# Kernel tuning notes

Measured on AMD Instinct MI355X. Metric: run time of the kernel, lower is better.

The kernel has to match this reference:

```python
import jax, jax.numpy as jnp
import numpy as np
import math

N_NODES = 100000
N_EDGES = 1600000
IN_FEATS = 64
H_FEATS = 64
NUM_CLASSES = 2
LS_D = [2, 4, 6, 8]
LS_COEFF = [1.0, 1.0, 1.0, 1.0]
K = 4  # polynomial order per conv (len of each theta)


def _chi_theta(d, coeff):
    # Faithful port of calculate_theta_Chi for d > 0: fit chi-square-like
    # density on [0,2] with a degree-3 Chebyshev series, reverse coeffs.
    n = 2 * d
    m = 1.0 / (n / 2 + 1)  # i = n/2 - 1, m = 1/(i+2)
    def y(x):
        x = np.asarray(x, dtype=np.float64)
        return 1.0 / (2 ** (n / 2) * math.gamma(n / 2)) * (x / m) ** (n / 2 - 1) * np.exp(-(x / m) / 2)
    xs = np.linspace(0.0, 2.0, 20001)
    S = np.trapz(y(xs), xs)  # dense trapezoid ~ scipy.integrate.quad on [0,2]
    lambs = np.linspace(0.0, 2.0, 500)
    c = np.polynomial.chebyshev.chebfit(lambs, y(lambs) / S, 3)
    return (c[::-1] * coeff).astype(np.float32)

THETAS_NP = np.stack([_chi_theta(d, c) for d, c in zip(LS_D, LS_COEFF)])  # [4, K]


def setup_inputs() -> dict:
    key = jax.random.key(0)
    ks = jax.random.split(key, 8)
    sc = 0.05
    return {
        "x": jax.random.normal(ks[0], (N_NODES, IN_FEATS), dtype=jnp.float32),
        "src": jax.random.randint(ks[1], (N_EDGES,), 0, N_NODES, dtype=jnp.int32),
        "dst": jax.random.randint(ks[2], (N_EDGES,), 0, N_NODES, dtype=jnp.int32),
        "thetas": jnp.asarray(THETAS_NP),
        "W1": jax.random.normal(ks[3], (IN_FEATS, H_FEATS), dtype=jnp.float32) * sc,
        "b1": jnp.zeros((H_FEATS,), dtype=jnp.float32),
        "W2": jax.random.normal(ks[4], (H_FEATS, H_FEATS), dtype=jnp.float32) * sc,
        "b2": jnp.zeros((H_FEATS,), dtype=jnp.float32),
        "Wm1": jax.random.normal(ks[5], (H_FEATS * len(LS_D), H_FEATS), dtype=jnp.float32) * sc,
        "bm1": jnp.zeros((H_FEATS,), dtype=jnp.float32),
        "Wm2": jax.random.normal(ks[6], (H_FEATS, NUM_CLASSES), dtype=jnp.float32) * sc,
        "bm2": jnp.zeros((NUM_CLASSES,), dtype=jnp.float32),
    }


def reference(x, src, dst, thetas, W1, b1, W2, b2, Wm1, bm1, Wm2, bm2):
    n = x.shape[0]
    # input MLP stem
    h = jax.nn.relu(x @ W1 + b1)
    h = jax.nn.relu(h @ W2 + b2)
    # D^{-1/2} from in-degrees (clamped to >= 1), as in DGL in_degrees()
    deg = jax.ops.segment_sum(jnp.ones_like(dst, dtype=h.dtype), dst, num_segments=n)
    dinv = jnp.maximum(deg, 1.0) ** -0.5  # [N]
    dinv = dinv[:, None]  # [N, 1]
    # shared Laplacian power sequence: feats[k] = L^k h with L = I - D^-1/2 A D^-1/2
    feats = [h]
    f = h
    for _ in range(K - 1):
        t = f * dinv                                   # [N, H]
        agg = jax.ops.segment_sum(t[src], dst, num_segments=n)  # gather-scatter SpMM
        f = f - agg * dinv
        feats.append(f)
    F = jnp.stack(feats)  # [K, N, H]
    # per-conv polynomial combination, then concat along feature dim
    h_final = jnp.einsum('ck,knh->nch', thetas, F).reshape(n, -1)  # [N, C*H]
    # output MLP (2 layers)
    h_out = jax.nn.relu(h_final @ Wm1 + bm1)
    return h_out @ Wm2 + bm2
```

## Files before the change

### kernel.cpp

```cpp
#include <hip/hip_runtime.h>
#include <math.h>

#define TS  256
#define GS  192
#define BCAP2 4608
#define CHUNK 4096

typedef __attribute__((ext_vector_type(8))) short short8v;
typedef __attribute__((ext_vector_type(4))) float f32x4;

__device__ __forceinline__ unsigned short f2bf(float f) {
    unsigned int u = __builtin_bit_cast(unsigned int, f);
    u += 0x7fff + ((u >> 16) & 1);
    return (unsigned short)(u >> 16);
}
__device__ __forceinline__ float bf2f(unsigned short s) {
    return __builtin_bit_cast(float, ((unsigned int)s) << 16);
}
__device__ __forceinline__ void fma4(float4& a, float s, const float4& b) {
    a.x = fmaf(s, b.x, a.x);
    a.y = fmaf(s, b.y, a.y);
    a.z = fmaf(s, b.z, a.z);
    a.w = fmaf(s, b.w, a.w);
}

__global__ void zero_k(int* __restrict__ p, int n) {
    int i = blockIdx.x * blockDim.x + threadIdx.x;
    int st = gridDim.x * blockDim.x;
    for (; i < n; i += st) p[i] = 0;
}

__global__ __launch_bounds__(256) void part1_k(const int* __restrict__ src,
        const int* __restrict__ dst, int* __restrict__ gcnt,
        unsigned int* __restrict__ pairs, int E, int NB) {
    __shared__ int lcnt[512];
    __shared__ int lbase[512];
    __shared__ int lpos[512];
    int tid = threadIdx.x;
    int base = blockIdx.x * CHUNK;
    int m = E - base; if (m > CHUNK) m = CHUNK;
    for (int b = tid; b < NB; b += 256) { lcnt[b] = 0; lpos[b] = 0; }
    __syncthreads();
    for (int i = tid; i < m; i += 256)
        atomicAdd(&lcnt[dst[base + i] >> 8], 1);
    __syncthreads();
    for (int b = tid; b < NB; b += 256)
        lbase[b] = (lcnt[b] > 0) ? atomicAdd(&gcnt[b], lcnt[b]) : 0;
    __syncthreads();
    for (int i = tid; i < m; i += 256) {
        int s = src[base + i], d = dst[base + i];
        int b = d >> 8;
        int p = atomicAdd(&lpos[b], 1);
        int idx = lbase[b] + p;
        if (idx < BCAP2)
            pairs[(size_t)b * BCAP2 + idx] = (unsigned int)s | ((unsigned int)(d & 255) << 17);
    }
}

__global__ __launch_bounds__(512) void bscan_k(const int* __restrict__ gcnt,
        int* __restrict__ bbase, int* __restrict__ rowp, int NB, int E, int n) {
    __shared__ int buf[512];
    int tid = threadIdx.x;
    int v = (tid < NB) ? (gcnt[tid] > BCAP2 ? BCAP2 : gcnt[tid]) : 0;
    buf[tid] = v;
    __syncthreads();
    int x = v;
    for (int off = 1; off < 512; off <<= 1) {
        int t = (tid >= off) ? buf[tid - off] : 0;
        __syncthreads();
        x += t;
        buf[tid] = x;
        __syncthreads();
    }
    if (tid < NB) bbase[tid] = x - v;
    if (tid == 0) rowp[n] = E;
}

__global__ __launch_bounds__(256) void csr2_k(const int* __restrict__ gcnt,
        const unsigned int* __restrict__ pairs, const int* __restrict__ bbase,
        int* __restrict__ rowp, int* __restrict__ colb, float* __restrict__ dinv, int n) {
    int b = blockIdx.x;
    int tid = threadIdx.x;
    int cntb = gcnt[b]; if (cntb > BCAP2) cntb = BCAP2;
    const unsigned int* pb = pairs + (size_t)b * BCAP2;
    __shared__ int c[256];
    __shared__ int sc[256];
    __shared__ int lpos[256];
    c[tid] = 0; lpos[tid] = 0;
    __syncthreads();
    for (int i = tid; i < cntb; i += 256)
        atomicAdd(&c[pb[i] >> 17], 1);
    __syncthreads();
    int v = c[tid];
    sc[tid] = v;
    __syncthreads();
    int x = v;
    for (int off = 1; off < 256; off <<= 1) {
        int t = (tid >= off) ? sc[tid - off] : 0;
        __syncthreads();
        x += t;
        sc[tid] = x;
        __syncthreads();
    }
    int ex = x - v;
    sc[tid] = ex;
    int node = b * 256 + tid;
    if (node < n) {
        rowp[node] = bbase[b] + ex;
        dinv[node] = 1.0f / sqrtf((float)(v > 1 ? v : 1));
    }
    __syncthreads();
    for (int i = tid; i < cntb; i += 256) {
        unsigned int pk = pb[i];
        int j = pk >> 17;
        int p = atomicAdd(&lpos[j], 1);
        colb[bbase[b] + sc[j] + p] = (int)(pk & 0x1FFFF);
    }
}

__global__ __launch_bounds__(256) void mlp_k(const float* __restrict__ x,
        const float* __restrict__ W1, const float* __restrict__ b1,
        const float* __restrict__ W2, const float* __restrict__ b2,
        const float* __restrict__ dinv,
        unsigned short* __restrict__ Ghi, unsigned short* __restrict__ Glo,
        int n, int ntiles) {
    __shared__ float Ws1[64 * 64];
    __shared__ float Ws2[64 * 64];
    __shared__ float xT[64 * 68];
    int tid = threadIdx.x;
    int ti = tid >> 4, tj = tid & 15;
    for (int idx = tid; idx < 4096; idx += 256) { Ws1[idx] = W1[idx]; Ws2[idx] = W2[idx]; }
    float4 b1v = *(const float4*)&b1[4 * tj];
    float4 b2v = *(const float4*)&b2[4 * tj];

    for (int g = blockIdx.x; g < ntiles; g += gridDim.x) {
        int base = g * 64;
        __syncthreads();
        for (int it = 0; it < 4; it++) {
            int node = ti + it * 16;
            int gn = base + node;
            float4 v = make_float4(0.f, 0.f, 0.f, 0.f);
            if (gn < n) v = *(const float4*)&x[(size_t)gn * 64 + 4 * tj];
            xT[(4 * tj + 0) * 68 + node] = v.x;
            xT[(4 * tj + 1) * 68 + node] = v.y;
            xT[(4 * tj + 2) * 68 + node] = v.z;
            xT[(4 * tj + 3) * 68 + node] = v.w;
        }
        __syncthreads();

        float4 a0 = b1v, a1 = b1v, a2 = b1v, a3 = b1v;
        #pragma unroll 8
        for (int k = 0; k < 64; k++) {
            float4 xv = *(const float4*)&xT[k * 68 + 4 * ti];
            float4 wv = *(const float4*)&Ws1[k * 64 + 4 * tj];
            fma4(a0, xv.x, wv); fma4(a1, xv.y, wv); fma4(a2, xv.z, wv); fma4(a3, xv.w, wv);
        }
        __syncthreads();
        {
            int hb = (4 * tj) * 68 + 4 * ti;
            xT[hb + 0 * 68 + 0] = fmaxf(a0.x, 0.f);
            xT[hb + 1 * 68 + 0] = fmaxf(a0.y, 0.f);
            xT[hb + 2 * 68 + 0] = fmaxf(a0.z, 0.f);
            xT[hb + 3 * 68 + 0] = fmaxf(a0.w, 0.f);
            xT[hb + 0 * 68 + 1] = fmaxf(a1.x, 0.f);
            xT[hb + 1 * 68 + 1] = fmaxf(a1.y, 0.f);
            xT[hb + 2 * 68 + 1] = fmaxf(a1.z, 0.f);
            xT[hb + 3 * 68 + 1] = fmaxf(a1.w, 0.f);
            xT[hb + 0 * 68 + 2] = fmaxf(a2.x, 0.f);
            xT[hb + 1 * 68 + 2] = fmaxf(a2.y, 0.f);
            xT[hb + 2 * 68 + 2] = fmaxf(a2.z, 0.f);
            xT[hb + 3 * 68 + 2] = fmaxf(a2.w, 0.f);
            xT[hb + 0 * 68 + 3] = fmaxf(a3.x, 0.f);
            xT[hb + 1 * 68 + 3] = fmaxf(a3.y, 0.f);
            xT[hb + 2 * 68 + 3] = fmaxf(a3.z, 0.f);
            xT[hb + 3 * 68 + 3] = fmaxf(a3.w, 0.f);
        }
        __syncthreads();

        a0 = b2v; a1 = b2v; a2 = b2v; a3 = b2v;
        #pragma unroll 8
        for (int k = 0; k < 64; k++) {
            float4 xv = *(const float4*)&xT[k * 68 + 4 * ti];
            float4 wv = *(const float4*)&Ws2[k * 64 + 4 * tj];
            fma4(a0, xv.x, wv); fma4(a1, xv.y, wv); fma4(a2, xv.z, wv); fma4(a3, xv.w, wv);
        }
        int gn0 = base + 4 * ti;
#define STORE_ROW(ai, ii)                                                                  \
        {                                                                                  \
            int gn = gn0 + (ii);                                                           \
            if (gn < n) {                                                                  \
                float dg = dinv[gn];                                                       \
                float g0 = fmaxf(ai.x, 0.f) * dg, g1 = fmaxf(ai.y, 0.f) * dg;              \
                float g2 = fmaxf(ai.z, 0.f) * dg, g3 = fmaxf(ai.w, 0.f) * dg;              \
                ushort4 hv, lv;                                                            \
                hv.x = f2bf(g0); lv.x = f2bf(g0 - bf2f(hv.x));                             \
                hv.y = f2bf(g1); lv.y = f2bf(g1 - bf2f(hv.y));                             \
                hv.z = f2bf(g2); lv.z = f2bf(g2 - bf2f(hv.z));                             \
                hv.w = f2bf(g3); lv.w = f2bf(g3 - bf2f(hv.w));                             \
                *(ushort4*)&Ghi[(size_t)gn * TS + 4 * tj] = hv;                            \
                *(ushort4*)&Glo[(size_t)gn * GS + 4 * tj] = lv;                            \
            }                                                                              \
        }
        STORE_ROW(a0, 0) STORE_ROW(a1, 1) STORE_ROW(a2, 2) STORE_ROW(a3, 3)
#undef STORE_ROW
    }
}

__global__ void wm1p_k(const float* __restrict__ thetas, const float* __restrict__ Wm1,
                       unsigned short* __restrict__ Wth, unsigned short* __restrict__ Wtl) {
    int idx = blockIdx.x * blockDim.x + threadIdx.x;
    if (idx >= 16384) return;
    int j = idx & 63;
    int q = idx >> 6;
    int k = q >> 6;
    int hh = q & 63;
    float a = 0.f;
    for (int c = 0; c < 4; c++) a += thetas[c * 4 + k] * Wm1[(c * 64 + hh) * 64 + j];
    unsigned short hi = f2bf(a);
    float r = a - bf2f(hi);
    Wth[j * 256 + q] = hi;
    Wtl[j * 256 + q] = f2bf(r);
}

__global__ __launch_bounds__(256) void prop_k(
        const unsigned short* __restrict__ TinHi,
        const unsigned short* __restrict__ TinLo,
        unsigned short* __restrict__ ToutHi,
        unsigned short* __restrict__ ToutLo,
        const int* __restrict__ rowp, const int* __restrict__ colb,
        const float* __restrict__ dinv, int n, int writeLo) {
    int w = (blockIdx.x * blockDim.x + threadIdx.x) >> 6;
    int lane = threadIdx.x & 63;
    int nA = 2 * w, nB = 2 * w + 1;
    if (nA >= n) return;
    bool hasB = (nB < n);
    int eA = rowp[nA], endA = rowp[nA + 1];
    int eB = 0, endB = 0;
    if (hasB) { eB = rowp[nB]; endB = rowp[nB + 1]; }
    float a0 = 0.f, a1 = 0.f, b0 = 0.f, b1 = 0.f;
    while (eA + 7 < endA && eB + 7 < endB) {
        int sA0 = colb[eA],     sA1 = colb[eA + 1], sA2 = colb[eA + 2], sA3 = colb[eA + 3];
        int sA4 = colb[eA + 4], sA5 = colb[eA + 5], sA6 = colb[eA + 6], sA7 = colb[eA + 7];
        int sB0 = colb[eB],     sB1 = colb[eB + 1], sB2 = colb[eB + 2], sB3 = colb[eB + 3];
        int sB4 = colb[eB + 4], sB5 = colb[eB + 5], sB6 = colb[eB + 6], sB7 = colb[eB + 7];
        float fA0 = bf2f(TinHi[(size_t)sA0 * TS + lane]);
        float fA1 = bf2f(TinHi[(size_t)sA1 * TS + lane]);
        float fA2 = bf2f(TinHi[(size_t)sA2 * TS + lane]);
        float fA3 = bf2f(TinHi[(size_t)sA3 * TS + lane]);
        float fA4 = bf2f(TinHi[(size_t)sA4 * TS + lane]);
        float fA5 = bf2f(TinHi[(size_t)sA5 * TS + lane]);
        float fA6 = bf2f(TinHi[(size_t)sA6 * TS + lane]);
        float fA7 = bf2f(TinHi[(size_t)sA7 * TS + lane]);
        float fB0 = bf2f(TinHi[(size_t)sB0 * TS + lane]);
        float fB1 = bf2f(TinHi[(size_t)sB1 * TS + lane]);
        float fB2 = bf2f(TinHi[(size_t)sB2 * TS + lane]);
        float fB3 = bf2f(TinHi[(size_t)sB3 * TS + lane]);
        float fB4 = bf2f(TinHi[(size_t)sB4 * TS + lane]);
        float fB5 = bf2f(TinHi[(size_t)sB5 * TS + lane]);
        float fB6 = bf2f(TinHi[(size_t)sB6 * TS + lane]);
        float fB7 = bf2f(TinHi[(size_t)sB7 * TS + lane]);
        a0 += (fA0 + fA2) + (fA4 + fA6);
        a1 += (fA1 + fA3) + (fA5 + fA7);
        b0 += (fB0 + fB2) + (fB4 + fB6);
        b1 += (fB1 + fB3) + (fB5 + fB7);
        eA += 8; eB += 8;
    }
    while (eA + 3 < endA) {
        int s0 = colb[eA], s1 = colb[eA + 1], s2 = colb[eA + 2], s3 = colb[eA + 3];
        float f0 = bf2f(TinHi[(size_t)s0 * TS + lane]);
        float f1 = bf2f(TinHi[(size_t)s1 * TS + lane]);
        float f2 = bf2f(TinHi[(size_t)s2 * TS + lane]);
        float f3 = bf2f(TinHi[(size_t)s3 * TS + lane]);
        a0 += f0 + f2; a1 += f1 + f3;
        eA += 4;
    }
    while (eB + 3 < endB) {
        int s0 = colb[eB], s1 = colb[eB + 1], s2 = colb[eB + 2], s3 = colb[eB + 3];
        float f0 = bf2f(TinHi[(size_t)s0 * TS + lane]);
        float f1 = bf2f(TinHi[(size_t)s1 * TS + lane]);
        float f2 = bf2f(TinHi[(size_t)s2 * TS + lane]);
        float f3 = bf2f(TinHi[(size_t)s3 * TS + lane]);
        b0 += f0 + f2; b1 += f1 + f3;
        eB += 4;
    }
    for (; eA < endA; ++eA) a0 += bf2f(TinHi[(size_t)colb[eA] * TS + lane]);
    for (; eB < endB; ++eB) b0 += bf2f(TinHi[(size_t)colb[eB] * TS + lane]);

    {
        float acc = a0 + a1;
        float dg = dinv[nA];
        float gin = bf2f(TinHi[(size_t)nA * TS + lane]) + bf2f(TinLo[(size_t)nA * GS + lane]);
        float go = gin - dg * dg * acc;
        unsigned short hi = f2bf(go);
        ToutHi[(size_t)nA * TS + lane] = hi;
        if (writeLo) ToutLo[(size_t)nA * GS + lane] = f2bf(go - bf2f(hi));
    }
    if (hasB) {
        float acc = b0 + b1;
        float dg = dinv[nB];
        float gin = bf2f(TinHi[(size_t)nB * TS + lane]) + bf2f(TinLo[(size_t)nB * GS + lane]);
        float go = gin - dg * dg * acc;
        unsigned short hi = f2bf(go);
        ToutHi[(size_t)nB * TS + lane] = hi;
        if (writeLo) ToutLo[(size_t)nB * GS + lane] = f2bf(go - bf2f(hi));
    }
}

__global__ __launch_bounds__(512, 4) void final_k(const unsigned short* __restrict__ Tcat,
        const float* __restrict__ dinv,
        const unsigned short* __restrict__ Wth, const unsigned short* __restrict__ Wtl,
        const float* __restrict__ bm1, const float* __restrict__ Wm2,
        const float* __restrict__ bm2, float* __restrict__ out, int n) {
    __shared__ float Lp[4][128][2];
    int tid = threadIdx.x;
    int w = tid >> 6, l = tid & 63;
    int cw = w & 3, half = w >> 2;
    int colg = 16 * cw + (l & 15);
    int krow = (l >> 4) * 8;

    short8v bhi[8], blo[8];
    #pragma unroll
    for (int ks = 0; ks < 8; ks++) {
        bhi[ks] = *(const short8v*)&Wth[colg * 256 + ks * 32 + krow];
        blo[ks] = *(const short8v*)&Wtl[colg * 256 + ks * 32 + krow];
    }
    float bm1c = bm1[colg];
    float w2x = Wm2[colg * 2 + 0], w2y = Wm2[colg * 2 + 1];

    int gbase = blockIdx.x * 128 + half * 64;
    const unsigned short* abase = &Tcat[(size_t)(gbase + (l & 15)) * TS + krow];

    for (int rt = 0; rt < 4; rt++) {
        f32x4 acc = {0.f, 0.f, 0.f, 0.f};
        const unsigned short* ap = abase + (size_t)rt * 16 * TS;
        #pragma unroll
        for (int ks = 0; ks < 8; ks++) {
            short8v a = *(const short8v*)(ap + ks * 32);
            acc = __builtin_amdgcn_mfma_f32_16x16x32_bf16(a, bhi[ks], acc, 0, 0, 0);
            acc = __builtin_amdgcn_mfma_f32_16x16x32_bf16(a, blo[ks], acc, 0, 0, 0);
        }
        #pragma unroll
        for (int i = 0; i < 4; i++) {
            int rl = half * 64 + rt * 16 + (l >> 4) * 4 + i;
            int grow = blockIdx.x * 128 + rl;
            float s = (grow < n) ? (1.0f / dinv[grow]) : 0.f;
            float h = fmaxf(fmaf(acc[i], s, bm1c), 0.f);
            float q0 = h * w2x, q1 = h * w2y;
            q0 += __shfl_xor(q0, 1); q1 += __shfl_xor(q1, 1);
            q0 += __shfl_xor(q0, 2); q1 += __shfl_xor(q1, 2);
            q0 += __shfl_xor(q0, 4); q1 += __shfl_xor(q1, 4);
            q0 += __shfl_xor(q0, 8); q1 += __shfl_xor(q1, 8);
            if ((l & 15) == 0) {
                Lp[cw][rl][0] = q0;
                Lp[cw][rl][1] = q1;
            }
        }
    }
    __syncthreads();
    if (tid < 256) {
        int r = tid >> 1, ch = tid & 1;
        int grow = blockIdx.x * 128 + r;
        if (grow < n) {
            float v = Lp[0][r][ch] + Lp[1][r][ch] + Lp[2][r][ch] + Lp[3][r][ch] + bm2[ch];
            out[grow * 2 + ch] = v;
        }
    }
}

extern "C" void kernel_launch(void* const* d_in, const int* in_sizes, int n_in,
                              void* d_out, int out_size, void* d_ws, size_t ws_size,
                              hipStream_t stream) {
    const float* x      = (const float*)d_in[0];
    const int*   src    = (const int*)d_in[1];
    const int*   dst    = (const int*)d_in[2];
    const float* thetas = (const float*)d_in[3];
    const float* W1     = (const float*)d_in[4];
    const float* b1     = (const float*)d_in[5];
    const float* W2     = (const float*)d_in[6];
    const float* b2     = (const float*)d_in[7];
    const float* Wm1    = (const float*)d_in[8];
    const float* bm1    = (const float*)d_in[9];
    const float* Wm2    = (const float*)d_in[10];
    const float* bm2    = (const float*)d_in[11];
    float* out = (float*)d_out;

    int n = in_sizes[0] / 64;
    int E = in_sizes[1];
    int ntiles  = (n + 63) / 64;
    int ntiles2 = (n + 127) / 128;
    int NB = (n + 255) / 256;

    unsigned short* Glo = (unsigned short*)d_ws;
    float* dinv  = (float*)(Glo + (size_t)n * GS);
    int*   rowp  = (int*)(dinv + n);
    int*   colb  = rowp + (n + 1);
    size_t woff = (((size_t)(colb + E) - (size_t)d_ws) + 15) & ~(size_t)15;
    unsigned short* Wth = (unsigned short*)((char*)d_ws + woff);
    unsigned short* Wtl = Wth + 16384;
    int*   gcnt  = (int*)(Wtl + 16384);
    int*   bbase = gcnt + NB;
    size_t uoff = (((size_t)(bbase + NB) - (size_t)d_ws) + 255) & ~(size_t)255;
    unsigned int*   pairs = (unsigned int*)((char*)d_ws + uoff);
    unsigned short* Ghi   = (unsigned short*)pairs;

    int nchunksP = (E + CHUNK - 1) / CHUNK;

    zero_k<<<4, 256, 0, stream>>>(gcnt, NB);
    part1_k<<<nchunksP, 256, 0, stream>>>(src, dst, gcnt, pairs, E, NB);
    bscan_k<<<1, 512, 0, stream>>>(gcnt, bbase, rowp, NB, E, n);
    csr2_k<<<NB, 256, 0, stream>>>(gcnt, pairs, bbase, rowp, colb, dinv, n);

    mlp_k<<<768, 256, 0, stream>>>(x, W1, b1, W2, b2, dinv, Ghi, Glo, n, ntiles);
    wm1p_k<<<64, 256, 0, stream>>>(thetas, Wm1, Wth, Wtl);

    int nwaves = (n + 1) / 2;
    int pblocks = ((size_t)nwaves * 64 + 255) / 256;
    prop_k<<<pblocks, 256, 0, stream>>>(
        Ghi + 0 * 64, Glo + 0 * 64, Ghi + 1 * 64, Glo + 1 * 64, rowp, colb, dinv, n, 1);
    prop_k<<<pblocks, 256, 0, stream>>>(
        Ghi + 1 * 64, Glo + 1 * 64, Ghi + 2 * 64, Glo + 2 * 64, rowp, colb, dinv, n, 1);
    prop_k<<<pblocks, 256, 0, stream>>>(
        Ghi + 2 * 64, Glo + 2 * 64, Ghi + 3 * 64, Glo + 2 * 64, rowp, colb, dinv, n, 0);

    final_k<<<ntiles2, 512, 0, stream>>>(Ghi, dinv, Wth, Wtl, bm1, Wm2, bm2, out, n);
}
```

Baseline: 290.8 us.

## Make final_k persistent with LDS-staged swizzled weight and activation tiles

```diff
diff --git a/kernel.cpp b/kernel.cpp
--- a/kernel.cpp
+++ b/kernel.cpp
@@ -306,63 +306,85 @@
     }
 }
 
-__global__ __launch_bounds__(512, 4) void final_k(const unsigned short* __restrict__ Tcat,
+__global__ __launch_bounds__(512) void final_k(const unsigned short* __restrict__ Ghi,
         const float* __restrict__ dinv,
         const unsigned short* __restrict__ Wth, const unsigned short* __restrict__ Wtl,
         const float* __restrict__ bm1, const float* __restrict__ Wm2,
-        const float* __restrict__ bm2, float* __restrict__ out, int n) {
+        const float* __restrict__ bm2, float* __restrict__ out, int n, int ntiles) {
+    __shared__ unsigned short Bs[32768];
+    __shared__ unsigned short As[32768];
     __shared__ float Lp[4][128][2];
     int tid = threadIdx.x;
     int w = tid >> 6, l = tid & 63;
     int cw = w & 3, half = w >> 2;
     int colg = 16 * cw + (l & 15);
-    int krow = (l >> 4) * 8;
-
-    short8v bhi[8], blo[8];
-    #pragma unroll
-    for (int ks = 0; ks < 8; ks++) {
-        bhi[ks] = *(const short8v*)&Wth[colg * 256 + ks * 32 + krow];
-        blo[ks] = *(const short8v*)&Wtl[colg * 256 + ks * 32 + krow];
+    int grp = l >> 4;
+
+    for (int i = tid; i < 4096; i += 512) {
+        int byte = i * 16;
+        int col = byte >> 9;
+        int swz = byte ^ ((col & 7) << 4);
+        uint4 v = (byte < 32768) ? *(const uint4*)((const char*)Wth + byte)
+                                 : *(const uint4*)((const char*)Wtl + (byte - 32768));
+        *(uint4*)((char*)Bs + swz) = v;
     }
     float bm1c = bm1[colg];
     float w2x = Wm2[colg * 2 + 0], w2y = Wm2[colg * 2 + 1];
-
-    int gbase = blockIdx.x * 128 + half * 64;
-    const unsigned short* abase = &Tcat[(size_t)(gbase + (l & 15)) * TS + krow];
-
-    for (int rt = 0; rt < 4; rt++) {
-        f32x4 acc = {0.f, 0.f, 0.f, 0.f};
-        const unsigned short* ap = abase + (size_t)rt * 16 * TS;
-        #pragma unroll
-        for (int ks = 0; ks < 8; ks++) {
-            short8v a = *(const short8v*)(ap + ks * 32);
-            acc = __builtin_amdgcn_mfma_f32_16x16x32_bf16(a, bhi[ks], acc, 0, 0, 0);
-            acc = __builtin_amdgcn_mfma_f32_16x16x32_bf16(a, blo[ks], acc, 0, 0, 0);
-        }
-        #pragma unroll
-        for (int i = 0; i < 4; i++) {
-            int rl = half * 64 + rt * 16 + (l >> 4) * 4 + i;
-            int grow = blockIdx.x * 128 + rl;
-            float s = (grow < n) ? (1.0f / dinv[grow]) : 0.f;
-            float h = fmaxf(fmaf(acc[i], s, bm1c), 0.f);
-            float q0 = h * w2x, q1 = h * w2y;
-            q0 += __shfl_xor(q0, 1); q1 += __shfl_xor(q1, 1);
-            q0 += __shfl_xor(q0, 2); q1 += __shfl_xor(q1, 2);
-            q0 += __shfl_xor(q0, 4); q1 += __shfl_xor(q1, 4);
-            q0 += __shfl_xor(q0, 8); q1 += __shfl_xor(q1, 8);
-            if ((l & 15) == 0) {
-                Lp[cw][rl][0] = q0;
-                Lp[cw][rl][1] = q1;
+    float bo0 = bm2[0], bo1 = bm2[1];
+    __syncthreads();
+
+    for (int g = blockIdx.x; g < ntiles; g += gridDim.x) {
+        const char* asrc = (const char*)(Ghi + (size_t)g * 128 * TS);
+        for (int i = tid; i < 4096; i += 512) {
+            int byte = i * 16;
+            int row = byte >> 9;
+            int swz = byte ^ ((row & 7) << 4);
+            *(uint4*)((char*)As + swz) = *(const uint4*)(asrc + byte);
+        }
+        __syncthreads();
+
+        for (int rt = 0; rt < 4; rt++) {
+            int arow = half * 64 + rt * 16 + (l & 15);
+            int abase = arow * 512 + grp * 16;
+            int axor = (arow & 7) << 4;
+            int bbase = colg * 512 + grp * 16;
+            int bxor = (colg & 7) << 4;
+            f32x4 acc = {0.f, 0.f, 0.f, 0.f};
+            #pragma unroll
+            for (int ks = 0; ks < 8; ks++) {
+                short8v a  = *(const short8v*)((const char*)As + ((abase + ks * 64) ^ axor));
+                int bb = (bbase + ks * 64) ^ bxor;
+                short8v bh = *(const short8v*)((const char*)Bs + bb);
+                short8v bl = *(const short8v*)((const char*)Bs + (bb + 32768));
+                acc = __builtin_amdgcn_mfma_f32_16x16x32_bf16(a, bh, acc, 0, 0, 0);
+                acc = __builtin_amdgcn_mfma_f32_16x16x32_bf16(a, bl, acc, 0, 0, 0);
             }
-        }
-    }
-    __syncthreads();
-    if (tid < 256) {
-        int r = tid >> 1, ch = tid & 1;
-        int grow = blockIdx.x * 128 + r;
-        if (grow < n) {
-            float v = Lp[0][r][ch] + Lp[1][r][ch] + Lp[2][r][ch] + Lp[3][r][ch] + bm2[ch];
-            out[grow * 2 + ch] = v;
+            #pragma unroll
+            for (int i = 0; i < 4; i++) {
+                int rl = half * 64 + rt * 16 + (l >> 4) * 4 + i;
+                int grow = g * 128 + rl;
+                float s = (grow < n) ? (1.0f / dinv[grow]) : 0.f;
+                float h = fmaxf(fmaf(acc[i], s, bm1c), 0.f);
+                float q0 = h * w2x, q1 = h * w2y;
+                q0 += __shfl_xor(q0, 1); q1 += __shfl_xor(q1, 1);
+                q0 += __shfl_xor(q0, 2); q1 += __shfl_xor(q1, 2);
+                q0 += __shfl_xor(q0, 4); q1 += __shfl_xor(q1, 4);
+                q0 += __shfl_xor(q0, 8); q1 += __shfl_xor(q1, 8);
+                if ((l & 15) == 0) {
+                    Lp[cw][rl][0] = q0;
+                    Lp[cw][rl][1] = q1;
+                }
+            }
+        }
+        __syncthreads();
+        if (tid < 256) {
+            int r = tid >> 1, ch = tid & 1;
+            int grow = g * 128 + r;
+            if (grow < n) {
+                float v = Lp[0][r][ch] + Lp[1][r][ch] + Lp[2][r][ch] + Lp[3][r][ch]
+                        + ((ch == 0) ? bo0 : bo1);
+                out[grow * 2 + ch] = v;
+            }
         }
     }
 }
@@ -422,5 +444,6 @@
     prop_k<<<pblocks, 256, 0, stream>>>(
         Ghi + 2 * 64, Glo + 2 * 64, Ghi + 3 * 64, Glo + 2 * 64, rowp, colb, dinv, n, 0);
 
-    final_k<<<ntiles2, 512, 0, stream>>>(Ghi, dinv, Wth, Wtl, bm1, Wm2, bm2, out, n);
-}
+    int fgrid = ntiles2 < 256 ? ntiles2 : 256;
+    final_k<<<fgrid, 512, 0, stream>>>(Ghi, dinv, Wth, Wtl, bm1, Wm2, bm2, out, n, ntiles2);
+}
```

New measurement: 277.3 us. 4.6% less time.
